# Optimization experiments

Hardware: AMD Instinct MI355X
Metric: run time of the kernel (lower is better)

## Reference

```python
import jax, jax.numpy as jnp
import numpy as np
import math

DIMS = [2048, 1024, 512, 4096]
NH, DK, DV = 16, 64, 64
BS = 8192
D_MODEL = NH * DK  # 1024


def setup_inputs() -> dict:
    key = jax.random.key(0)
    ks = jax.random.split(key, 3 * len(DIMS) + 5)
    inp = {"input_data": jax.random.normal(ks[0], (BS, sum(DIMS)), jnp.float32)}
    ki = 1
    for i, d in enumerate(DIMS):
        inp[f"wq{i}"] = jax.random.normal(ks[ki], (NH * DK, d), jnp.float32) * 0.02; ki += 1
        inp[f"wk{i}"] = jax.random.normal(ks[ki], (NH * DK, d), jnp.float32) * 0.02; ki += 1
        inp[f"wv{i}"] = jax.random.normal(ks[ki], (NH * DV, d), jnp.float32) * 0.02; ki += 1
    inp["fc_w"] = jax.random.normal(ks[ki], (NH * DV, NH * DV), jnp.float32) * 0.02; ki += 1
    inp["fc_b"] = jax.random.normal(ks[ki], (NH * DV,), jnp.float32) * 0.02; ki += 1
    inp["ln_g"] = jnp.ones((NH * DV,), jnp.float32)
    inp["ln_b"] = jnp.zeros((NH * DV,), jnp.float32)
    return inp


def _forward(input_data, wqs, wks, wvs, fc_w, fc_b, ln_g, ln_b):
    bs = input_data.shape[0]
    M = len(DIMS)
    offs = np.cumsum([0] + DIMS)
    # per-modality projections; stack into [bs, M, NH*D]
    xs = [input_data[:, offs[i]:offs[i + 1]] for i in range(M)]
    q = jnp.stack([x @ w.T for x, w in zip(xs, wqs)], axis=1)  # [bs, M, NH*DK]
    k = jnp.stack([x @ w.T for x, w in zip(xs, wks)], axis=1)
    v = jnp.stack([x @ w.T for x, w in zip(xs, wvs)], axis=1)  # [bs, M, NH*DV]
    residual = v  # v.transpose(1,2).view == original stacked v
    qh = q.reshape(bs, M, NH, DK).transpose(0, 2, 1, 3)  # [bs, NH, M, DK]
    kh = k.reshape(bs, M, NH, DK).transpose(0, 2, 1, 3)
    vh = v.reshape(bs, M, NH, DV).transpose(0, 2, 1, 3)
    scores = jnp.einsum('bhqd,bhkd->bhqk', qh, kh) / math.sqrt(DK)
    attn = jax.nn.softmax(scores, axis=-1)  # [bs, NH, M, M]
    ctx = jnp.einsum('bhqk,bhkd->bhqd', attn, vh)  # [bs, NH, M, DV]
    ctx = ctx.transpose(0, 2, 1, 3).reshape(bs, M, NH * DV)
    out = ctx @ fc_w.T + fc_b  # dropout is identity (p=0 / eval)
    out = out + residual
    mu = jnp.mean(out, axis=-1, keepdims=True)
    var = jnp.var(out, axis=-1, keepdims=True)
    out = (out - mu) / jnp.sqrt(var + 1e-6) * ln_g + ln_b
    return out, attn


def reference(input_data, wq0, wk0, wv0, wq1, wk1, wv1, wq2, wk2, wv2,
              wq3, wk3, wv3, fc_w, fc_b, ln_g, ln_b):
    wqs = [wq0, wq1, wq2, wq3]
    wks = [wk0, wk1, wk2, wk3]
    wvs = [wv0, wv1, wv2, wv3]
    return _forward(input_data, wqs, wks, wvs, fc_w, fc_b, ln_g, ln_b)
```

## Files before the change

### kernel.cpp

```cpp
#include <hip/hip_runtime.h>


typedef unsigned short u16;
typedef short short8 __attribute__((ext_vector_type(8)));
typedef unsigned short u16x4 __attribute__((ext_vector_type(4)));
typedef float f32x4 __attribute__((ext_vector_type(4)));

__device__ __forceinline__ u16 f2bf(float f) {
  unsigned u = __builtin_bit_cast(unsigned, f);
  u += 0x7FFFu + ((u >> 16) & 1u);
  return (u16)(u >> 16);
}
__device__ __forceinline__ float bf2f(u16 s) {
  return __builtin_bit_cast(float, ((unsigned)s) << 16);
}

__device__ __forceinline__ void gload16(const u16* g, u16* l) {
  __builtin_amdgcn_global_load_lds(
      (const __attribute__((address_space(1))) void*)g,
      (__attribute__((address_space(3))) void*)l, 16, 0, 0);
}

#define CFENCE asm volatile("" ::: "memory")

struct CArgs {
  const float* src[14];
  unsigned long dst[14];
  int blk0[14];
  int n4[14];
};

__global__ __launch_bounds__(256) void convall(CArgs a, u16* __restrict__ wsb) {
  int blk = blockIdx.x;
  int s = 0;
#pragma unroll
  for (int i = 1; i < 14; ++i) s = (blk >= a.blk0[i]) ? i : s;
  int li = (blk - a.blk0[s]) * 256 + threadIdx.x;
  if (li < a.n4[s]) {
    f32x4 v = __builtin_nontemporal_load((const f32x4*)a.src[s] + li);
    u16x4 o;
    o.x = f2bf(v.x); o.y = f2bf(v.y); o.z = f2bf(v.z); o.w = f2bf(v.w);
    *((u16x4*)(wsb + a.dst[s]) + li) = o;
  }
}

template <int MODE>
__global__ __launch_bounds__(512, 2)
void gemm8(const u16* __restrict__ Abase, int lda,
           const u16* __restrict__ Wbase, u16* __restrict__ Cq,
           u16* __restrict__ Cpre, const float* __restrict__ bias,
           const u16* __restrict__ resid) {
  __shared__ __align__(16) u16 lds[65536];

  const int tid = threadIdx.x;
  const int w = tid >> 6, lane = tid & 63;
  const int lr = lane & 15, lk = lane >> 4;
  const int wm = w >> 2, wn = w & 3;

  int K, nt, bx, by, coff;
  const u16 *A, *B;
  if (MODE == 0) {
    int seg = blockIdx.x / 384;
    int r = blockIdx.x % 384;
    bx = r % 12; by = r / 12;
    K = 4096 >> seg; nt = 64 >> seg;
    int xo, wo, mod;
    switch (seg) {
      case 0:  xo = 3584; wo = 11010048; mod = 3; break;
      case 1:  xo = 0;    wo = 0;        mod = 0; break;
      case 2:  xo = 2048; wo = 6291456;  mod = 1; break;
      default: xo = 3072; wo = 9437184;  mod = 2; break;
    }
    coff = mod * 3072;
    A = Abase + xo;
    B = Wbase + wo;
  } else {
    bx = blockIdx.x & 3; by = blockIdx.x >> 2;
    K = 1024; nt = 16; coff = 0;
    A = Abase; B = Wbase;
  }
  const size_t brow = (size_t)by * 256;
  const int bcol = bx * 256;
  const u16* Ab = A + brow * (size_t)lda;
  const u16* Bb = B + (size_t)bcol * (size_t)K;

  f32x4 acc[8][4];
#pragma unroll
  for (int i = 0; i < 8; ++i)
#pragma unroll
    for (int j = 0; j < 4; ++j) acc[i][j] = (f32x4){0.f, 0.f, 0.f, 0.f};

  auto stageA = [&](int p, int half) {
    const int base = (p & 1) * 65536 + half * 16384;
    const int k0 = p * 64;
#pragma unroll
    for (int l = 0; l < 2; ++l) {
      int s = l * 8192 + tid * 16;
      int rw = s >> 7;
      int ck = ((s >> 4) & 7) ^ (rw & 7);
      int row = (rw & 63) + ((rw >> 6) << 7) + half * 64;
      gload16(Ab + (size_t)row * lda + k0 + ck * 8, &lds[(base + s) >> 1]);
    }
  };
  auto stageB = [&](int p, int half) {
    const int base = (p & 1) * 65536 + 32768 + half * 16384;
    const int k0 = p * 64;
#pragma unroll
    for (int l = 0; l < 2; ++l) {
      int s = l * 8192 + tid * 16;
      int rw = s >> 7;
      int ck = ((s >> 4) & 7) ^ (rw & 7);
      int col = (rw & 31) + ((rw >> 5) << 6) + half * 32;
      gload16(Bb + (size_t)col * (size_t)K + k0 + ck * 8, &lds[(base + s) >> 1]);
    }
  };

  auto ldA = [&](int t, int half, short8* dst) {
    const u16* lp = lds + (((t & 1) * 65536 + half * 16384) >> 1);
#pragma unroll
    for (int mi = 0; mi < 4; ++mi) {
      int rw = wm * 64 + mi * 16 + lr;
#pragma unroll
      for (int ks = 0; ks < 2; ++ks) {
        int pc = (ks * 4 + lk) ^ (rw & 7);
        dst[mi * 2 + ks] = *(const short8*)(lp + rw * 64 + pc * 8);
      }
    }
  };
  auto ldB = [&](int t, int half, short8* dst) {
    const u16* lp = lds + (((t & 1) * 65536 + 32768 + half * 16384) >> 1);
#pragma unroll
    for (int ni = 0; ni < 2; ++ni) {
      int rw = wn * 32 + ni * 16 + lr;
#pragma unroll
      for (int ks = 0; ks < 2; ++ks) {
        int pc = (ks * 4 + lk) ^ (rw & 7);
        dst[ni * 2 + ks] = *(const short8*)(lp + rw * 64 + pc * 8);
      }
    }
  };

  short8 af[8], bl[4], bh[4];
  auto MQ = [&](short8* a, short8* b, int mo, int no) {
#pragma unroll
    for (int mi = 0; mi < 4; ++mi)
#pragma unroll
      for (int ni = 0; ni < 2; ++ni) {
        acc[mo + mi][no + ni] = __builtin_amdgcn_mfma_f32_16x16x32_bf16(
            a[mi * 2 + 0], b[ni * 2 + 0], acc[mo + mi][no + ni], 0, 0, 0);
        acc[mo + mi][no + ni] = __builtin_amdgcn_mfma_f32_16x16x32_bf16(
            a[mi * 2 + 1], b[ni * 2 + 1], acc[mo + mi][no + ni], 0, 0, 0);
      }
  };

  stageA(0, 0); stageB(0, 0); stageB(0, 1); stageA(0, 1);
  asm volatile("s_waitcnt vmcnt(4)" ::: "memory");
  __builtin_amdgcn_s_barrier();
  CFENCE;

#pragma unroll 1
  for (int t = 0; t < nt; ++t) {
    const bool more = (t + 1 < nt);
    ldA(t, 0, af);
    ldB(t, 0, bl);
    if (more) { stageA(t + 1, 0); stageB(t + 1, 0); }
    CFENCE;
    __builtin_amdgcn_s_barrier();
    asm volatile("s_waitcnt lgkmcnt(0)" ::: "memory");
    __builtin_amdgcn_sched_barrier(0);
    __builtin_amdgcn_s_setprio(1);
    MQ(af, bl, 0, 0);
    __builtin_amdgcn_s_setprio(0);
    CFENCE;
    if (more) asm volatile("s_waitcnt vmcnt(4)" ::: "memory");
    else      asm volatile("s_waitcnt vmcnt(0)" ::: "memory");
    __builtin_amdgcn_s_barrier();
    CFENCE;
    ldB(t, 1, bh);
    CFENCE;
    __builtin_amdgcn_s_barrier();
    asm volatile("s_waitcnt lgkmcnt(0)" ::: "memory");
    __builtin_amdgcn_sched_barrier(0);
    __builtin_amdgcn_s_setprio(1);
    MQ(af, bh, 0, 2);
    __builtin_amdgcn_s_setprio(0);
    CFENCE;
    __builtin_amdgcn_s_barrier();
    CFENCE;
    ldA(t, 1, af);
    if (more) { stageB(t + 1, 1); stageA(t + 1, 1); }
    CFENCE;
    __builtin_amdgcn_s_barrier();
    asm volatile("s_waitcnt lgkmcnt(0)" ::: "memory");
    __builtin_amdgcn_sched_barrier(0);
    __builtin_amdgcn_s_setprio(1);
    MQ(af, bh, 4, 2);
    __builtin_amdgcn_s_setprio(0);
    CFENCE;
    __builtin_amdgcn_s_barrier();
    CFENCE;
    __builtin_amdgcn_s_setprio(1);
    MQ(af, bl, 4, 0);
    __builtin_amdgcn_s_setprio(0);
    CFENCE;
    if (more) {
      asm volatile("s_waitcnt vmcnt(4)" ::: "memory");
      __builtin_amdgcn_s_barrier();
      CFENCE;
    }
  }

  if (MODE == 0) {
#pragma unroll
    for (int mi = 0; mi < 8; ++mi)
#pragma unroll
      for (int ni = 0; ni < 4; ++ni) {
        const int c = coff + bcol + wn * 64 + ni * 16 + lr;
#pragma unroll
        for (int j = 0; j < 4; ++j) {
          size_t r = brow + wm * 128 + mi * 16 + lk * 4 + j;
          Cq[r * 12288 + c] = f2bf(acc[mi][ni][j]);
        }
      }
  } else {
#pragma unroll
    for (int mi = 0; mi < 8; ++mi)
#pragma unroll
      for (int ni = 0; ni < 4; ++ni) {
        const int c = bcol + wn * 64 + ni * 16 + lr;
        const float bs = bias[c];
#pragma unroll
        for (int j = 0; j < 4; ++j) {
          size_t r = brow + wm * 128 + mi * 16 + lk * 4 + j;
          size_t ridx = (r >> 2) * 12288 + (r & 3) * 3072 + 2048 + c;
          Cpre[r * 1024 + c] = f2bf(acc[mi][ni][j] + bs + bf2f(resid[ridx]));
        }
      }
  }
}

__global__ __launch_bounds__(256) void attn_k(const u16* __restrict__ qkv,
                                              u16* __restrict__ ctxb,
                                              float* __restrict__ attn_out) {
  const int tid = threadIdx.x;
  const int l = tid & 63;
  const int wg = blockIdx.x * 4 + (tid >> 6);
  const int b = wg >> 2;
  const int h0 = (wg & 3) << 2;
  const size_t base = (size_t)b * 12288 + h0 * 64 + l * 4;

  float q[4][4], k[4][4], v[4][4];
#pragma unroll
  for (int m = 0; m < 4; ++m) {
    u16x4 uq = __builtin_nontemporal_load((const u16x4*)(qkv + base + m * 3072));
    u16x4 uk = __builtin_nontemporal_load((const u16x4*)(qkv + base + m * 3072 + 1024));
    u16x4 uv = __builtin_nontemporal_load((const u16x4*)(qkv + base + m * 3072 + 2048));
    q[m][0] = bf2f(uq.x); q[m][1] = bf2f(uq.y); q[m][2] = bf2f(uq.z); q[m][3] = bf2f(uq.w);
    k[m][0] = bf2f(uk.x); k[m][1] = bf2f(uk.y); k[m][2] = bf2f(uk.z); k[m][3] = bf2f(uk.w);
    v[m][0] = bf2f(uv.x); v[m][1] = bf2f(uv.y); v[m][2] = bf2f(uv.z); v[m][3] = bf2f(uv.w);
  }

  float s[16];
#pragma unroll
  for (int i = 0; i < 4; ++i)
#pragma unroll
    for (int j = 0; j < 4; ++j) {
      float acc = q[i][0] * k[j][0];
      acc += q[i][1] * k[j][1];
      acc += q[i][2] * k[j][2];
      acc += q[i][3] * k[j][3];
      s[i * 4 + j] = acc;
    }
#pragma unroll
  for (int off = 1; off < 16; off <<= 1) {
#pragma unroll
    for (int t = 0; t < 16; ++t) s[t] += __shfl_xor(s[t], off);
  }

  float a[16];
#pragma unroll
  for (int i = 0; i < 4; ++i) {
    float s0 = s[i * 4 + 0] * 0.125f, s1 = s[i * 4 + 1] * 0.125f;
    float s2 = s[i * 4 + 2] * 0.125f, s3 = s[i * 4 + 3] * 0.125f;
    float m = fmaxf(fmaxf(s0, s1), fmaxf(s2, s3));
    float e0 = __expf(s0 - m), e1 = __expf(s1 - m);
    float e2 = __expf(s2 - m), e3 = __expf(s3 - m);
    float inv = 1.0f / (e0 + e1 + e2 + e3);
    a[i * 4 + 0] = e0 * inv; a[i * 4 + 1] = e1 * inv;
    a[i * 4 + 2] = e2 * inv; a[i * 4 + 3] = e3 * inv;
  }

#pragma unroll
  for (int i = 0; i < 4; ++i) {
    float c0 = a[i*4+0]*v[0][0] + a[i*4+1]*v[1][0] + a[i*4+2]*v[2][0] + a[i*4+3]*v[3][0];
    float c1 = a[i*4+0]*v[0][1] + a[i*4+1]*v[1][1] + a[i*4+2]*v[2][1] + a[i*4+3]*v[3][1];
    float c2 = a[i*4+0]*v[0][2] + a[i*4+1]*v[1][2] + a[i*4+2]*v[2][2] + a[i*4+3]*v[3][2];
    float c3 = a[i*4+0]*v[0][3] + a[i*4+1]*v[1][3] + a[i*4+2]*v[2][3] + a[i*4+3]*v[3][3];
    u16x4 o;
    o.x = f2bf(c0); o.y = f2bf(c1); o.z = f2bf(c2); o.w = f2bf(c3);
    *(u16x4*)(ctxb + (size_t)b * 4096 + i * 1024 + h0 * 64 + l * 4) = o;
  }

  int sel = l & 15;
  float val = a[0];
#pragma unroll
  for (int t = 1; t < 16; ++t) val = (sel == t) ? a[t] : val;
  __builtin_nontemporal_store(val, &attn_out[(size_t)b * 256 + h0 * 16 + l]);
}

__global__ __launch_bounds__(256) void ln_k(const u16* __restrict__ pre,
                                            const float* __restrict__ g,
                                            const float* __restrict__ b,
                                            float* __restrict__ out) {
  int row = blockIdx.x;
  int tid = threadIdx.x;
  u16x4 u = __builtin_nontemporal_load(
      (const u16x4*)(pre + (size_t)row * 1024 + tid * 4));
  float x0 = bf2f(u.x), x1 = bf2f(u.y), x2 = bf2f(u.z), x3 = bf2f(u.w);
  float s = x0 + x1 + x2 + x3;
  float s2 = x0 * x0 + x1 * x1 + x2 * x2 + x3 * x3;
#pragma unroll
  for (int off = 32; off; off >>= 1) {
    s += __shfl_xor(s, off);
    s2 += __shfl_xor(s2, off);
  }
  __shared__ float r1[4], r2[4];
  int w = tid >> 6, lane = tid & 63;
  if (lane == 0) { r1[w] = s; r2[w] = s2; }
  __syncthreads();
  s = r1[0] + r1[1] + r1[2] + r1[3];
  s2 = r2[0] + r2[1] + r2[2] + r2[3];
  float mu = s * (1.0f / 1024.0f);
  float inv = rsqrtf(s2 * (1.0f / 1024.0f) - mu * mu + 1e-6f);
  float4 gv = *(const float4*)(g + tid * 4);
  float4 bv = *(const float4*)(b + tid * 4);
  f32x4 o;
  o.x = (x0 - mu) * inv * gv.x + bv.x;
  o.y = (x1 - mu) * inv * gv.y + bv.y;
  o.z = (x2 - mu) * inv * gv.z + bv.z;
  o.w = (x3 - mu) * inv * gv.w + bv.w;
  __builtin_nontemporal_store(o, (f32x4*)(out + (size_t)row * 1024 + tid * 4));
}

extern "C" void kernel_launch(void* const* d_in, const int* in_sizes, int n_in,
                              void* d_out, int out_size, void* d_ws,
                              size_t ws_size, hipStream_t stream) {
  const float* fcb = (const float*)d_in[14];
  const float* lng = (const float*)d_in[15];
  const float* lnb = (const float*)d_in[16];

  u16* wsb = (u16*)d_ws;
  u16* xb = wsb;
  u16* wb = xb + 62914560;
  u16* qkv = wb + 24641536;
  u16* ctxb = qkv + 100663296;
  u16* pre = wsb;
  float* outp = (float*)d_out;
  float* attn_out = outp + 33554432;

  static const unsigned long woff[13] = {
      0,        2097152,  4194304,
      6291456,  7340032,  8388608,
      9437184,  9961472,  10485760,
      11010048, 15204352, 19398656,
      23592960};
  static const int wn4[13] = {524288, 524288, 524288, 262144, 262144, 262144,
                              131072, 131072, 131072, 1048576, 1048576, 1048576,
                              262144};

  CArgs ca;
  ca.src[0] = (const float*)d_in[0];
  ca.dst[0] = 0;
  ca.n4[0] = 62914560 / 4;
  ca.blk0[0] = 0;
  int nb = ca.n4[0] / 256;
  for (int i = 0; i < 13; ++i) {
    ca.src[i + 1] = (const float*)d_in[1 + i];
    ca.dst[i + 1] = 62914560ul + woff[i];
    ca.n4[i + 1] = wn4[i];
    ca.blk0[i + 1] = nb;
    nb += (wn4[i] + 255) / 256;
  }
  convall<<<dim3(nb), 256, 0, stream>>>(ca, wsb);

  gemm8<0><<<dim3(1536), 512, 0, stream>>>(xb, 7680, wb, qkv, nullptr, nullptr,
                                           nullptr);

  attn_k<<<dim3(8192), 256, 0, stream>>>(qkv, ctxb, attn_out);

  gemm8<1><<<dim3(512), 512, 0, stream>>>(ctxb, 1024, wb + 23592960, nullptr,
                                          pre, fcb, qkv);

  ln_k<<<dim3(32768), 256, 0, stream>>>(pre, lng, lnb, outp);
}
```

Before: 609.6 us.

## Load B fragments directly from global into registers, triple-buffer A in LDS

The GEMM main loop now stages only the A tile through LDS, using a 4-slot ring with prefetch distance two. Each wave loads its B operand fragments straight from global memory into registers, double-buffered across iterations, which removes the B LDS staging and the half-tile barriers. The aim is to cut LDS traffic and synchronization per K step. In exchange, each wave issues uncoalesced, strided global reads of B (only 16 bytes per row per lane), raises register pressure, and fixes the waitcnt counts by hand. The unrolled loop also assumes nt is even.

```diff
diff --git a/kernel.cpp b/kernel.cpp
--- a/kernel.cpp
+++ b/kernel.cpp
@@ -84,130 +84,82 @@
   const u16* Ab = A + brow * (size_t)lda;
   const u16* Bb = B + (size_t)bcol * (size_t)K;
 
+  const u16* bp0 = Bb + (size_t)(wn * 64 + 0 * 16 + lr) * (size_t)K + lk * 8;
+  const u16* bp1 = Bb + (size_t)(wn * 64 + 1 * 16 + lr) * (size_t)K + lk * 8;
+  const u16* bp2 = Bb + (size_t)(wn * 64 + 2 * 16 + lr) * (size_t)K + lk * 8;
+  const u16* bp3 = Bb + (size_t)(wn * 64 + 3 * 16 + lr) * (size_t)K + lk * 8;
+
   f32x4 acc[8][4];
 #pragma unroll
   for (int i = 0; i < 8; ++i)
 #pragma unroll
     for (int j = 0; j < 4; ++j) acc[i][j] = (f32x4){0.f, 0.f, 0.f, 0.f};
 
-  auto stageA = [&](int p, int half) {
-    const int base = (p & 1) * 65536 + half * 16384;
+  auto stageA = [&](int p) {
+    const int base = (p & 3) * 32768;
     const int k0 = p * 64;
 #pragma unroll
-    for (int l = 0; l < 2; ++l) {
+    for (int l = 0; l < 4; ++l) {
       int s = l * 8192 + tid * 16;
       int rw = s >> 7;
       int ck = ((s >> 4) & 7) ^ (rw & 7);
-      int row = (rw & 63) + ((rw >> 6) << 7) + half * 64;
-      gload16(Ab + (size_t)row * lda + k0 + ck * 8, &lds[(base + s) >> 1]);
+      gload16(Ab + (size_t)rw * lda + k0 + ck * 8, &lds[(base + s) >> 1]);
     }
   };
-  auto stageB = [&](int p, int half) {
-    const int base = (p & 1) * 65536 + 32768 + half * 16384;
-    const int k0 = p * 64;
-#pragma unroll
-    for (int l = 0; l < 2; ++l) {
-      int s = l * 8192 + tid * 16;
-      int rw = s >> 7;
-      int ck = ((s >> 4) & 7) ^ (rw & 7);
-      int col = (rw & 31) + ((rw >> 5) << 6) + half * 32;
-      gload16(Bb + (size_t)col * (size_t)K + k0 + ck * 8, &lds[(base + s) >> 1]);
+
+  auto loadB = [&](int t, short8* dst) {
+    const int ko = t * 64;
+#pragma unroll
+    for (int ks = 0; ks < 2; ++ks) {
+      dst[0 * 2 + ks] = *(const short8*)(bp0 + ko + ks * 32);
+      dst[1 * 2 + ks] = *(const short8*)(bp1 + ko + ks * 32);
+      dst[2 * 2 + ks] = *(const short8*)(bp2 + ko + ks * 32);
+      dst[3 * 2 + ks] = *(const short8*)(bp3 + ko + ks * 32);
     }
   };
 
-  auto ldA = [&](int t, int half, short8* dst) {
-    const u16* lp = lds + (((t & 1) * 65536 + half * 16384) >> 1);
-#pragma unroll
-    for (int mi = 0; mi < 4; ++mi) {
-      int rw = wm * 64 + mi * 16 + lr;
-#pragma unroll
-      for (int ks = 0; ks < 2; ++ks) {
-        int pc = (ks * 4 + lk) ^ (rw & 7);
-        dst[mi * 2 + ks] = *(const short8*)(lp + rw * 64 + pc * 8);
-      }
-    }
+  auto body = [&](int s, short8* Bc, short8* Bn) {
+    if (s + 2 < nt) stageA(s + 2);
+    if (s + 1 < nt) loadB(s + 1, Bn);
+    CFENCE;
+    const u16* lp = lds + ((s & 3) * 32768 >> 1);
+#pragma unroll
+    for (int mi = 0; mi < 8; ++mi) {
+      const int rw = wm * 128 + mi * 16 + lr;
+      const u16* rp = lp + rw * 64;
+      short8 a0 = *(const short8*)(rp + ((0 * 4 + lk) ^ (rw & 7)) * 8);
+      short8 a1 = *(const short8*)(rp + ((1 * 4 + lk) ^ (rw & 7)) * 8);
+#pragma unroll
+      for (int ni = 0; ni < 4; ++ni)
+        acc[mi][ni] = __builtin_amdgcn_mfma_f32_16x16x32_bf16(
+            a0, Bc[ni * 2 + 0], acc[mi][ni], 0, 0, 0);
+#pragma unroll
+      for (int ni = 0; ni < 4; ++ni)
+        acc[mi][ni] = __builtin_amdgcn_mfma_f32_16x16x32_bf16(
+            a1, Bc[ni * 2 + 1], acc[mi][ni], 0, 0, 0);
+    }
+    CFENCE;
+    if (s + 2 < nt) {
+      asm volatile("s_waitcnt vmcnt(20)" ::: "memory");
+      __builtin_amdgcn_s_barrier();
+    } else if (s + 1 < nt) {
+      asm volatile("s_waitcnt vmcnt(16)" ::: "memory");
+      __builtin_amdgcn_s_barrier();
+    }
+    CFENCE;
   };
-  auto ldB = [&](int t, int half, short8* dst) {
-    const u16* lp = lds + (((t & 1) * 65536 + 32768 + half * 16384) >> 1);
-#pragma unroll
-    for (int ni = 0; ni < 2; ++ni) {
-      int rw = wn * 32 + ni * 16 + lr;
-#pragma unroll
-      for (int ks = 0; ks < 2; ++ks) {
-        int pc = (ks * 4 + lk) ^ (rw & 7);
-        dst[ni * 2 + ks] = *(const short8*)(lp + rw * 64 + pc * 8);
-      }
-    }
-  };
-
-  short8 af[8], bl[4], bh[4];
-  auto MQ = [&](short8* a, short8* b, int mo, int no) {
-#pragma unroll
-    for (int mi = 0; mi < 4; ++mi)
-#pragma unroll
-      for (int ni = 0; ni < 2; ++ni) {
-        acc[mo + mi][no + ni] = __builtin_amdgcn_mfma_f32_16x16x32_bf16(
-            a[mi * 2 + 0], b[ni * 2 + 0], acc[mo + mi][no + ni], 0, 0, 0);
-        acc[mo + mi][no + ni] = __builtin_amdgcn_mfma_f32_16x16x32_bf16(
-            a[mi * 2 + 1], b[ni * 2 + 1], acc[mo + mi][no + ni], 0, 0, 0);
-      }
-  };
-
-  stageA(0, 0); stageB(0, 0); stageB(0, 1); stageA(0, 1);
-  asm volatile("s_waitcnt vmcnt(4)" ::: "memory");
+
+  short8 B0[8], B1[8];
+  stageA(0); stageA(1);
+  loadB(0, B0);
+  asm volatile("s_waitcnt vmcnt(0)" ::: "memory");
   __builtin_amdgcn_s_barrier();
   CFENCE;
 
 #pragma unroll 1
-  for (int t = 0; t < nt; ++t) {
-    const bool more = (t + 1 < nt);
-    ldA(t, 0, af);
-    ldB(t, 0, bl);
-    if (more) { stageA(t + 1, 0); stageB(t + 1, 0); }
-    CFENCE;
-    __builtin_amdgcn_s_barrier();
-    asm volatile("s_waitcnt lgkmcnt(0)" ::: "memory");
-    __builtin_amdgcn_sched_barrier(0);
-    __builtin_amdgcn_s_setprio(1);
-    MQ(af, bl, 0, 0);
-    __builtin_amdgcn_s_setprio(0);
-    CFENCE;
-    if (more) asm volatile("s_waitcnt vmcnt(4)" ::: "memory");
-    else      asm volatile("s_waitcnt vmcnt(0)" ::: "memory");
-    __builtin_amdgcn_s_barrier();
-    CFENCE;
-    ldB(t, 1, bh);
-    CFENCE;
-    __builtin_amdgcn_s_barrier();
-    asm volatile("s_waitcnt lgkmcnt(0)" ::: "memory");
-    __builtin_amdgcn_sched_barrier(0);
-    __builtin_amdgcn_s_setprio(1);
-    MQ(af, bh, 0, 2);
-    __builtin_amdgcn_s_setprio(0);
-    CFENCE;
-    __builtin_amdgcn_s_barrier();
-    CFENCE;
-    ldA(t, 1, af);
-    if (more) { stageB(t + 1, 1); stageA(t + 1, 1); }
-    CFENCE;
-    __builtin_amdgcn_s_barrier();
-    asm volatile("s_waitcnt lgkmcnt(0)" ::: "memory");
-    __builtin_amdgcn_sched_barrier(0);
-    __builtin_amdgcn_s_setprio(1);
-    MQ(af, bh, 4, 2);
-    __builtin_amdgcn_s_setprio(0);
-    CFENCE;
-    __builtin_amdgcn_s_barrier();
-    CFENCE;
-    __builtin_amdgcn_s_setprio(1);
-    MQ(af, bl, 4, 0);
-    __builtin_amdgcn_s_setprio(0);
-    CFENCE;
-    if (more) {
-      asm volatile("s_waitcnt vmcnt(4)" ::: "memory");
-      __builtin_amdgcn_s_barrier();
-      CFENCE;
-    }
+  for (int t = 0; t < nt; t += 2) {
+    body(t, B0, B1);
+    body(t + 1, B1, B0);
   }
 
   if (MODE == 0) {
```

Measured after the change: 805.8 us. 1.32x slower.
